# Kernel tuning notes

Hardware: AMD Instinct MI355X
Metric: run time of the kernel (lower is better)

## Reference

```python
import jax, jax.numpy as jnp
import numpy as np

N_TOK = 256
C_Z = 128
C = 32
N_HEAD = 4


def setup_inputs() -> dict:
    key = jax.random.key(0)
    ks = jax.random.split(key, 8)
    s = 0.02
    return {
        "z": jax.random.normal(ks[0], (N_TOK, N_TOK, C_Z), dtype=jnp.float32),
        "single_mask": jnp.ones((N_TOK,), dtype=jnp.float32),
        "ln_gamma": jnp.ones((C_Z,), dtype=jnp.float32),
        "ln_beta": jnp.zeros((C_Z,), dtype=jnp.float32),
        "W_q": jax.random.normal(ks[1], (C_Z, N_HEAD * C), dtype=jnp.float32) * s,
        "W_k": jax.random.normal(ks[2], (C_Z, N_HEAD * C), dtype=jnp.float32) * s,
        "W_v": jax.random.normal(ks[3], (C_Z, N_HEAD * C), dtype=jnp.float32) * s,
        "W_b": jax.random.normal(ks[4], (C_Z, N_HEAD), dtype=jnp.float32) * s,
        "W_g": jax.random.normal(ks[5], (C_Z, N_HEAD * C), dtype=jnp.float32) * s,
        "W_out": jax.random.normal(ks[6], (N_HEAD * C, C_Z), dtype=jnp.float32) * s,
    }


def reference(z, single_mask, ln_gamma, ln_beta, W_q, W_k, W_v, W_b, W_g, W_out):
    # LayerNorm over c_z
    mu = jnp.mean(z, axis=-1, keepdims=True)
    var = jnp.var(z, axis=-1, keepdims=True)
    zn = (z - mu) * jax.lax.rsqrt(var + 1e-5) * ln_gamma + ln_beta

    n = zn.shape[0]
    proj = lambda W: (zn @ W).reshape(n, n, N_HEAD, C)
    q = proj(W_q)
    k = proj(W_k)
    v = proj(W_v)
    g = proj(W_g)
    b = zn @ W_b  # [i, j, h] -> used as bias b[j, k, h]

    # a[i,j,k,h] = q[i,j]·k[i,k]/sqrt(c) + b[j,k,h]
    a = jnp.einsum('ijhc,ikhc->ijkh', q, k) / np.sqrt(C).astype(np.float32)
    a = a + b[None, :, :, :]
    a = a + (-1e9) * (1.0 - single_mask)[None, None, :, None]
    a = jax.nn.softmax(a, axis=-2)  # over k

    o = jnp.einsum('ijkh,ikhc->ijhc', a, v)
    o = jax.nn.sigmoid(g) * o
    o = o.reshape(n, n, N_HEAD * C)
    return o @ W_out
```

## Files before the change

kernel.cpp:

```cpp
#include <hip/hip_runtime.h>
#include <hip/hip_bf16.h>

#define NT 256
#define CZ 128
#define CH 32
#define NH 4
#define PL 2097152

typedef unsigned short ushort_t;
typedef unsigned int uint_t;
typedef __attribute__((ext_vector_type(8))) short short8;
typedef __attribute__((ext_vector_type(4))) float f32x4;

__device__ __forceinline__ float bfbits2f(uint_t bits){
  union { uint_t u; float f; } v; v.u = bits; return v.f;
}
__device__ __forceinline__ float bf2f(ushort_t u){
  return bfbits2f(((uint_t)u) << 16);
}
__device__ __forceinline__ ushort_t f2bf(float f){
  union { float f; uint_t u; } v; v.f = f;
  uint_t u = v.u;
  uint_t r = (u + 0x7fffu + ((u >> 16) & 1u)) >> 16;
  return (ushort_t)r;
}
__device__ __forceinline__ void unpk(uint_t w, float& lo, float& hi){
  lo = bfbits2f(w << 16);
  hi = bfbits2f(w & 0xffff0000u);
}
__device__ __forceinline__ short8 as_s8(uint4 u){
  union { uint4 u; short8 s; } v; v.u = u; return v.s;
}
__device__ __forceinline__ uint_t pk2(float a, float b){
  union { __hip_bfloat16 h; ushort_t u; } x, y;
  x.h = __float2bfloat16(a); y.h = __float2bfloat16(b);
  return (uint_t)x.u | ((uint_t)y.u << 16);
}
__device__ __forceinline__ int detect_f32(const ushort_t* zz){
  int l = threadIdx.x & 63;
  int bad = 0;
  #pragma unroll
  for(int s=0;s<4;s++){
    float v = bf2f(zz[l*4 + s]);
    if(!(fabsf(v) < 1e9f)) bad = 1;
  }
  return (__ballot(bad) != 0ull) ? 1 : 0;
}

__global__ __launch_bounds__(256) void k_cvt_wt(const void* __restrict__ s0,
    const void* __restrict__ s1, const void* __restrict__ s2,
    const void* __restrict__ s3, const void* __restrict__ s4,
    ushort_t* __restrict__ dst, const ushort_t* __restrict__ zz,
    const void* __restrict__ m_, const void* __restrict__ g_,
    const void* __restrict__ b_, const void* __restrict__ wb_,
    float* __restrict__ smallf){
  int isf32 = detect_f32(zz);
  if(blockIdx.x >= 320){
    int idx = threadIdx.x * 4;
    const void* sp; int off;
    if(idx < 256){ sp = m_;  off = idx; }
    else if(idx < 384){ sp = g_;  off = idx-256; }
    else if(idx < 512){ sp = b_;  off = idx-384; }
    else { sp = wb_; off = idx-512; }
    float4 o;
    if(isf32){ o = *(const float4*)((const float*)sp + off); }
    else {
      uint2 u = *(const uint2*)((const ushort_t*)sp + off);
      unpk(u.x, o.x, o.y); unpk(u.y, o.z, o.w);
    }
    *(float4*)(smallf + idx) = o;
    return;
  }
  const void* srcs[5] = {s0,s1,s2,s3,s4};
  int w = blockIdx.x >> 6;
  int idx = (blockIdx.x & 63)*256 + threadIdx.x;
  int k = idx >> 7, c = idx & 127;
  const void* sp = srcs[w];
  float v;
  if(isf32) v = ((const float*)sp)[idx];
  else      v = bf2f(((const ushort_t*)sp)[idx]);
  dst[(size_t)w*16384 + (size_t)c*128 + k] = f2bf(v);
}

__global__ __launch_bounds__(256) void k_lnproj(const void* __restrict__ zraw,
    const float* __restrict__ smallf, const ushort_t* __restrict__ Wt,
    ushort_t* __restrict__ qh, ushort_t* __restrict__ kh,
    ushort_t* __restrict__ vh, ushort_t* __restrict__ gh,
    float* __restrict__ btm){
  __shared__ __align__(16) char lds[37888];
  ushort_t* znl = (ushort_t*)lds;
  float*    wbs = (float*)(lds + 35840);
  const float* mkf = smallf;
  const float* gmf = smallf + 256;
  const float* btf = smallf + 384;
  const float* Wbf = smallf + 512;
  int t = threadIdx.x;
  int isf32 = detect_f32((const ushort_t*)zraw);
  wbs[t] = Wbf[t]; wbs[t+256] = Wbf[t+256];
  __syncthreads();

  int row_loc = t >> 1, half = t & 1;
  size_t r = (size_t)blockIdx.x*128 + row_loc;
  float mval = -1e9f * (1.f - mkf[r & 255]);
  float s = 0.f, s2 = 0.f;
  if(isf32){
    const float4* zp = (const float4*)((const float*)zraw + r*CZ + half*64);
    #pragma unroll
    for(int q=0;q<16;q++){
      float4 v = zp[q];
      s  += (v.x + v.y) + (v.z + v.w);
      s2 += (v.x*v.x + v.y*v.y) + (v.z*v.z + v.w*v.w);
    }
  } else {
    const uint4* zp = (const uint4*)((const ushort_t*)zraw + r*CZ + half*64);
    #pragma unroll
    for(int q=0;q<8;q++){
      uint4 u = zp[q];
      const uint_t* pu = (const uint_t*)&u;
      #pragma unroll
      for(int e=0;e<4;e++){
        float lo, hi; unpk(pu[e], lo, hi);
        s += lo + hi; s2 += lo*lo + hi*hi;
      }
    }
  }
  s  += __shfl_xor(s, 1);
  s2 += __shfl_xor(s2, 1);
  float mu  = s * (1.f/CZ);
  float var = fmaxf(s2 * (1.f/CZ) - mu*mu, 0.f);
  float rs  = rsqrtf(var + 1e-5f);
  float acch[4] = {0.f,0.f,0.f,0.f};
  #pragma unroll
  for(int chunk=0;chunk<8;chunk++){
    float v8[8];
    if(isf32){
      const float4* zp = (const float4*)((const float*)zraw + r*CZ + half*64 + chunk*8);
      float4 a = zp[0], b = zp[1];
      v8[0]=a.x; v8[1]=a.y; v8[2]=a.z; v8[3]=a.w;
      v8[4]=b.x; v8[5]=b.y; v8[6]=b.z; v8[7]=b.w;
    } else {
      uint4 u = *(const uint4*)((const ushort_t*)zraw + r*CZ + half*64 + chunk*8);
      const uint_t* pu = (const uint_t*)&u;
      #pragma unroll
      for(int e=0;e<4;e++) unpk(pu[e], v8[e*2], v8[e*2+1]);
    }
    uint_t ow[4];
    #pragma unroll
    for(int e2=0;e2<4;e2++){
      int cg = half*64 + chunk*8 + e2*2;
      float v0 = (v8[e2*2]   - mu)*rs*gmf[cg]   + btf[cg];
      float v1 = (v8[e2*2+1] - mu)*rs*gmf[cg+1] + btf[cg+1];
      float4 w0 = *(const float4*)&wbs[cg*4];
      float4 w1 = *(const float4*)&wbs[(cg+1)*4];
      acch[0] += v0*w0.x + v1*w1.x;
      acch[1] += v0*w0.y + v1*w1.y;
      acch[2] += v0*w0.z + v1*w1.z;
      acch[3] += v0*w0.w + v1*w1.w;
      ow[e2] = (uint_t)f2bf(v0) | ((uint_t)f2bf(v1) << 16);
    }
    uint4 o; o.x=ow[0]; o.y=ow[1]; o.z=ow[2]; o.w=ow[3];
    *(uint4*)(znl + row_loc*140 + half*64 + chunk*8) = o;
  }
  #pragma unroll
  for(int h=0;h<4;h++){
    float tot = acch[h] + __shfl_xor(acch[h], 1);
    if(half == 0) btm[(size_t)h*65536 + r] = (tot + mval) * 1.4426950408889634f;
  }
  __syncthreads();

  int wave = t>>6, l = t&63, n = l&15, quad = l>>4;
  uint4 af[2][4];
  #pragma unroll
  for(int mt=0;mt<2;mt++)
    #pragma unroll
    for(int kb=0;kb<4;kb++)
      af[mt][kb] = *(const uint4*)(znl + (wave*32 + mt*16 + n)*140 + kb*32 + quad*8);
  ushort_t* outs[4] = {qh, kh, vh, gh};
  size_t row0 = (size_t)blockIdx.x*128 + wave*32;
  #pragma unroll
  for(int w=0;w<4;w++){
    const ushort_t* W = Wt + (size_t)w*16384;
    ushort_t* D = outs[w];
    float sc = (w==0) ? (0.17677669529663687f * 1.4426950408889634f) : 1.f;
    #pragma unroll
    for(int nt=0;nt<8;nt++){
      uint4 bfr[4];
      #pragma unroll
      for(int kb=0;kb<4;kb++)
        bfr[kb] = *(const uint4*)(W + ((size_t)(nt*16 + n))*128 + kb*32 + quad*8);
      f32x4 a0 = {0.f,0.f,0.f,0.f}, a1 = {0.f,0.f,0.f,0.f};
      #pragma unroll
      for(int kb=0;kb<4;kb++){
        a0 = __builtin_amdgcn_mfma_f32_16x16x32_bf16(as_s8(bfr[kb]), as_s8(af[0][kb]), a0, 0,0,0);
        a1 = __builtin_amdgcn_mfma_f32_16x16x32_bf16(as_s8(bfr[kb]), as_s8(af[1][kb]), a1, 0,0,0);
      }
      uint2 s0p, s1p;
      s0p.x = pk2(a0[0]*sc, a0[1]*sc); s0p.y = pk2(a0[2]*sc, a0[3]*sc);
      s1p.x = pk2(a1[0]*sc, a1[1]*sc); s1p.y = pk2(a1[2]*sc, a1[3]*sc);
      ushort_t* Db = D + (size_t)(nt>>1)*PL + (size_t)(nt&1)*16 + quad*4;
      *(uint2*)(Db + (row0 + n)*CH)      = s0p;
      *(uint2*)(Db + (row0 + 16 + n)*CH) = s1p;
    }
  }
}

__global__ __launch_bounds__(512, 2) void k_attn(
    const ushort_t* __restrict__ qh, const ushort_t* __restrict__ kh,
    const ushort_t* __restrict__ vh, const ushort_t* __restrict__ gh,
    const float* __restrict__ btm, ushort_t* __restrict__ oh,
    const ushort_t* __restrict__ Wt4, void* __restrict__ outp,
    const ushort_t* __restrict__ zz){
  __shared__ __align__(16) char lds[147456];
  int t = threadIdx.x;
  int i = blockIdx.x;
  int w = t >> 6, l = t & 63;
  int h = w >> 1, sub = w & 1;
  int n = l & 15, quad = l >> 4;
  uint4*    Kf  = (uint4*)(lds + h*16384);
  uint4*    VfA = (uint4*)(lds + 65536 + h*16384);
  ushort_t* Pw  = (ushort_t*)(lds + 131072) + w*1024;
  const ushort_t* qhp = qh + (size_t)h*PL + (size_t)(i*NT)*CH;
  const ushort_t* khp = kh + (size_t)h*PL + (size_t)(i*NT)*CH;
  const ushort_t* vhp = vh + (size_t)h*PL + (size_t)(i*NT)*CH;
  const ushort_t* ghp = gh + (size_t)h*PL + (size_t)(i*NT)*CH;
  ushort_t*       ohp = oh + (size_t)h*PL + (size_t)(i*NT)*CH;
  const float*    bth = btm + (size_t)h*65536;

  {
    #pragma unroll
    for(int m=0;m<8;m++){
      int kt = sub*8 + m;
      Kf[kt*64 + l] = *(const uint4*)(khp + (size_t)(kt*16 + n)*CH + quad*8);
    }
  }
  {
    #pragma unroll
    for(int it=0; it<8; it++){
      int u = sub + it*2, kblk = u >> 1, ct = u & 1;
      uint_t d[4];
      #pragma unroll
      for(int e=0;e<4;e++){
        uint_t lo = vhp[(size_t)(kblk*32 + quad*8 + e*2    )*CH + ct*16 + n];
        uint_t hi = vhp[(size_t)(kblk*32 + quad*8 + e*2 + 1)*CH + ct*16 + n];
        d[e] = lo | (hi << 16);
      }
      uint4 o; o.x=d[0]; o.y=d[1]; o.z=d[2]; o.w=d[3];
      VfA[u*64 + l] = o;
    }
  }
  __syncthreads();

  int swz = (n & 7) << 4;

  #pragma unroll 1
  for(int s=0;s<8;s++){
    int jt = sub*8 + s;
    uint4 qf = *(const uint4*)(qhp + (size_t)(jt*16 + n)*CH + quad*8);
    f32x4 acc[16];
    #pragma unroll
    for(int kt=0;kt<16;kt++)
      acc[kt] = *(const f32x4*)(bth + (size_t)(jt*16 + n)*256 + kt*16 + quad*4);
    #pragma unroll
    for(int kt=0;kt<16;kt++){
      uint4 kfv = Kf[kt*64 + l];
      acc[kt] = __builtin_amdgcn_mfma_f32_16x16x32_bf16(as_s8(kfv), as_s8(qf), acc[kt], 0,0,0);
    }
    float sum0 = 0.f, sum1 = 0.f;
    f32x4 oa0 = {0.f,0.f,0.f,0.f}, oa1 = {0.f,0.f,0.f,0.f};
    #pragma unroll
    for(int H=0;H<2;H++){
      uint2 pv[8];
      #pragma unroll
      for(int kt=0;kt<8;kt++){
        float e0 = __builtin_amdgcn_exp2f(acc[H*8+kt][0]);
        float e1 = __builtin_amdgcn_exp2f(acc[H*8+kt][1]);
        float e2 = __builtin_amdgcn_exp2f(acc[H*8+kt][2]);
        float e3 = __builtin_amdgcn_exp2f(acc[H*8+kt][3]);
        sum0 += e0 + e1; sum1 += e2 + e3;
        pv[kt].x = pk2(e0, e1);
        pv[kt].y = pk2(e2, e3);
      }
      #pragma unroll
      for(int Q2=0;Q2<2;Q2++){
        #pragma unroll
        for(int m=0;m<4;m++)
          *(uint2*)((char*)Pw + (((n<<7) + (m<<5) + (quad<<3)) ^ swz)) = pv[Q2*4+m];
        #pragma unroll
        for(int kb=0;kb<2;kb++){
          uint4 pf = *(const uint4*)((char*)Pw + (((n<<7) + (kb<<6) + (quad<<4)) ^ swz));
          int kg = (H*2+Q2)*2 + kb;
          oa0 = __builtin_amdgcn_mfma_f32_16x16x32_bf16(as_s8(VfA[(kg*2+0)*64 + l]), as_s8(pf), oa0, 0,0,0);
          oa1 = __builtin_amdgcn_mfma_f32_16x16x32_bf16(as_s8(VfA[(kg*2+1)*64 + l]), as_s8(pf), oa1, 0,0,0);
        }
      }
    }
    float ssum = sum0 + sum1;
    ssum += __shfl_xor(ssum, 16);
    ssum += __shfl_xor(ssum, 32);
    float inv = 1.f / ssum;
    size_t rb = (size_t)(jt*16 + n)*CH;
    uint2 g0 = *(const uint2*)(ghp + rb + quad*4);
    uint2 g1 = *(const uint2*)(ghp + rb + 16 + quad*4);
    float ga[4], gc[4];
    unpk(g0.x, ga[0], ga[1]); unpk(g0.y, ga[2], ga[3]);
    unpk(g1.x, gc[0], gc[1]); unpk(g1.y, gc[2], gc[3]);
    float v0[4], v1[4];
    #pragma unroll
    for(int rr=0;rr<4;rr++){
      v0[rr] = oa0[rr] * inv * (1.f/(1.f + __expf(-ga[rr])));
      v1[rr] = oa1[rr] * inv * (1.f/(1.f + __expf(-gc[rr])));
    }
    uint2 s0, s1;
    s0.x = (uint_t)f2bf(v0[0]) | ((uint_t)f2bf(v0[1]) << 16);
    s0.y = (uint_t)f2bf(v0[2]) | ((uint_t)f2bf(v0[3]) << 16);
    s1.x = (uint_t)f2bf(v1[0]) | ((uint_t)f2bf(v1[1]) << 16);
    s1.y = (uint_t)f2bf(v1[2]) | ((uint_t)f2bf(v1[3]) << 16);
    *(uint2*)(ohp + rb + quad*4)      = s0;
    *(uint2*)(ohp + rb + 16 + quad*4) = s1;
  }
  __syncthreads();

  int isf32 = detect_f32(zz);
  size_t row0 = (size_t)i*NT + w*32;
  uint4 af[2][4];
  #pragma unroll
  for(int mt=0;mt<2;mt++)
    #pragma unroll
    for(int kb=0;kb<4;kb++)
      af[mt][kb] = *(const uint4*)(oh + (size_t)kb*PL + (row0 + mt*16 + n)*CH + quad*8);
  #pragma unroll
  for(int nt=0;nt<8;nt++){
    uint4 bfr[4];
    #pragma unroll
    for(int kb=0;kb<4;kb++)
      bfr[kb] = *(const uint4*)(Wt4 + ((size_t)(nt*16 + n))*128 + kb*32 + quad*8);
    f32x4 a0 = {0.f,0.f,0.f,0.f}, a1 = {0.f,0.f,0.f,0.f};
    #pragma unroll
    for(int kb=0;kb<4;kb++){
      a0 = __builtin_amdgcn_mfma_f32_16x16x32_bf16(as_s8(bfr[kb]), as_s8(af[0][kb]), a0, 0,0,0);
      a1 = __builtin_amdgcn_mfma_f32_16x16x32_bf16(as_s8(bfr[kb]), as_s8(af[1][kb]), a1, 0,0,0);
    }
    if(isf32){
      float* of = (float*)outp + nt*16 + quad*4;
      *(f32x4*)(of + (row0 + n)*CZ)      = a0;
      *(f32x4*)(of + (row0 + 16 + n)*CZ) = a1;
    } else {
      uint2 s0p, s1p;
      s0p.x = pk2(a0[0], a0[1]); s0p.y = pk2(a0[2], a0[3]);
      s1p.x = pk2(a1[0], a1[1]); s1p.y = pk2(a1[2], a1[3]);
      ushort_t* ob = (ushort_t*)outp + nt*16 + quad*4;
      *(uint2*)(ob + (row0 + n)*CZ)      = s0p;
      *(uint2*)(ob + (row0 + 16 + n)*CZ) = s1p;
    }
  }
}

extern "C" void kernel_launch(void* const* d_in, const int* in_sizes, int n_in,
                              void* d_out, int out_size, void* d_ws, size_t ws_size,
                              hipStream_t stream){
  char* wsb = (char*)d_ws;
  const size_t TB = (size_t)16777216;
  ushort_t* qh  = (ushort_t*)(wsb);
  ushort_t* kh  = (ushort_t*)(wsb + TB);
  ushort_t* vh  = (ushort_t*)(wsb + 2*TB);
  ushort_t* gh  = (ushort_t*)(wsb + 3*TB);
  ushort_t* oh  = (ushort_t*)(wsb + 4*TB);
  float*    btm = (float*)   (wsb + 5*TB);
  float*  smallf= (float*)   (wsb + 5*TB + (1u<<20));
  ushort_t* Wt  = (ushort_t*)(wsb + 5*TB + (1u<<20) + 4096);
  const ushort_t* zz = (const ushort_t*)d_in[0];

  k_cvt_wt   <<<321, 256, 0, stream>>>(d_in[4], d_in[5], d_in[6], d_in[8], d_in[9],
                                       Wt, zz, d_in[1], d_in[2], d_in[3], d_in[7], smallf);
  k_lnproj   <<<512, 256, 0, stream>>>(d_in[0], smallf, Wt, qh, kh, vh, gh, btm);
  k_attn     <<<256, 512, 0, stream>>>(qh, kh, vh, gh, btm, oh,
                                       Wt + (size_t)4*16384, d_out, zz);
}
```

Baseline: 197.5 us.

## Fuse LN and QKVG projection into attention kernel; split bias via folded LN algebra

After: 206.8 us. 1.05x slower.

```diff
diff --git a/kernel.cpp b/kernel.cpp
--- a/kernel.cpp
+++ b/kernel.cpp
@@ -53,7 +53,7 @@
     ushort_t* __restrict__ dst, const ushort_t* __restrict__ zz,
     const void* __restrict__ m_, const void* __restrict__ g_,
     const void* __restrict__ b_, const void* __restrict__ wb_,
-    float* __restrict__ smallf){
+    float* __restrict__ smallf, float* __restrict__ abct){
   int isf32 = detect_f32(zz);
   if(blockIdx.x >= 320){
     int idx = threadIdx.x * 4;
@@ -69,6 +69,21 @@
       unpk(u.x, o.x, o.y); unpk(u.y, o.z, o.w);
     }
     *(float4*)(smallf + idx) = o;
+    __syncthreads();
+    if(threadIdx.x < 128){
+      int c = threadIdx.x;
+      float g = smallf[256 + c];
+      #pragma unroll
+      for(int h=0;h<4;h++) abct[c*4 + h] = g * smallf[512 + c*4 + h];
+    }
+    if(threadIdx.x >= 128 && threadIdx.x < 136){
+      int k = threadIdx.x - 128;
+      int h = k & 3, which = k >> 2;
+      float acc = 0.f;
+      for(int c=0;c<128;c++)
+        acc += (which ? smallf[256 + c] : smallf[384 + c]) * smallf[512 + c*4 + h];
+      abct[512 + k] = acc;
+    }
     return;
   }
   const void* srcs[5] = {s0,s1,s2,s3,s4};
@@ -82,27 +97,21 @@
   dst[(size_t)w*16384 + (size_t)c*128 + k] = f2bf(v);
 }
 
-__global__ __launch_bounds__(256) void k_lnproj(const void* __restrict__ zraw,
-    const float* __restrict__ smallf, const ushort_t* __restrict__ Wt,
-    ushort_t* __restrict__ qh, ushort_t* __restrict__ kh,
-    ushort_t* __restrict__ vh, ushort_t* __restrict__ gh,
+__global__ __launch_bounds__(256) void k_bias(const void* __restrict__ zraw,
+    const float* __restrict__ smallf, const float* __restrict__ abct,
     float* __restrict__ btm){
-  __shared__ __align__(16) char lds[37888];
-  ushort_t* znl = (ushort_t*)lds;
-  float*    wbs = (float*)(lds + 35840);
-  const float* mkf = smallf;
-  const float* gmf = smallf + 256;
-  const float* btf = smallf + 384;
-  const float* Wbf = smallf + 512;
+  __shared__ float As[512];
+  __shared__ float BC[8];
   int t = threadIdx.x;
   int isf32 = detect_f32((const ushort_t*)zraw);
-  wbs[t] = Wbf[t]; wbs[t+256] = Wbf[t+256];
+  As[t] = abct[t]; As[t+256] = abct[t+256];
+  if(t < 8) BC[t] = abct[512 + t];
   __syncthreads();
-
   int row_loc = t >> 1, half = t & 1;
   size_t r = (size_t)blockIdx.x*128 + row_loc;
-  float mval = -1e9f * (1.f - mkf[r & 255]);
-  float s = 0.f, s2 = 0.f;
+  float mval = -1e9f * (1.f - smallf[r & 255]);
+  float s = 0.f, s2 = 0.f, d[4] = {0.f,0.f,0.f,0.f};
+  const float* Ah = As + half*256;
   if(isf32){
     const float4* zp = (const float4*)((const float*)zraw + r*CZ + half*64);
     #pragma unroll
@@ -110,6 +119,10 @@
       float4 v = zp[q];
       s  += (v.x + v.y) + (v.z + v.w);
       s2 += (v.x*v.x + v.y*v.y) + (v.z*v.z + v.w*v.w);
+      const float* a0 = Ah + q*16;
+      #pragma unroll
+      for(int h=0;h<4;h++)
+        d[h] += v.x*a0[h] + v.y*a0[4+h] + v.z*a0[8+h] + v.w*a0[12+h];
     }
   } else {
     const uint4* zp = (const uint4*)((const ushort_t*)zraw + r*CZ + half*64);
@@ -121,101 +134,139 @@
       for(int e=0;e<4;e++){
         float lo, hi; unpk(pu[e], lo, hi);
         s += lo + hi; s2 += lo*lo + hi*hi;
+        const float* a0 = Ah + (q*8 + e*2)*4;
+        #pragma unroll
+        for(int h=0;h<4;h++) d[h] += lo*a0[h] + hi*a0[4+h];
       }
     }
   }
   s  += __shfl_xor(s, 1);
   s2 += __shfl_xor(s2, 1);
-  float mu  = s * (1.f/CZ);
-  float var = fmaxf(s2 * (1.f/CZ) - mu*mu, 0.f);
-  float rs  = rsqrtf(var + 1e-5f);
-  float acch[4] = {0.f,0.f,0.f,0.f};
   #pragma unroll
-  for(int chunk=0;chunk<8;chunk++){
-    float v8[8];
-    if(isf32){
-      const float4* zp = (const float4*)((const float*)zraw + r*CZ + half*64 + chunk*8);
-      float4 a = zp[0], b = zp[1];
-      v8[0]=a.x; v8[1]=a.y; v8[2]=a.z; v8[3]=a.w;
-      v8[4]=b.x; v8[5]=b.y; v8[6]=b.z; v8[7]=b.w;
-    } else {
-      uint4 u = *(const uint4*)((const ushort_t*)zraw + r*CZ + half*64 + chunk*8);
-      const uint_t* pu = (const uint_t*)&u;
-      #pragma unroll
-      for(int e=0;e<4;e++) unpk(pu[e], v8[e*2], v8[e*2+1]);
-    }
-    uint_t ow[4];
-    #pragma unroll
-    for(int e2=0;e2<4;e2++){
-      int cg = half*64 + chunk*8 + e2*2;
-      float v0 = (v8[e2*2]   - mu)*rs*gmf[cg]   + btf[cg];
-      float v1 = (v8[e2*2+1] - mu)*rs*gmf[cg+1] + btf[cg+1];
-      float4 w0 = *(const float4*)&wbs[cg*4];
-      float4 w1 = *(const float4*)&wbs[(cg+1)*4];
-      acch[0] += v0*w0.x + v1*w1.x;
-      acch[1] += v0*w0.y + v1*w1.y;
-      acch[2] += v0*w0.z + v1*w1.z;
-      acch[3] += v0*w0.w + v1*w1.w;
-      ow[e2] = (uint_t)f2bf(v0) | ((uint_t)f2bf(v1) << 16);
-    }
-    uint4 o; o.x=ow[0]; o.y=ow[1]; o.z=ow[2]; o.w=ow[3];
-    *(uint4*)(znl + row_loc*140 + half*64 + chunk*8) = o;
-  }
-  #pragma unroll
-  for(int h=0;h<4;h++){
-    float tot = acch[h] + __shfl_xor(acch[h], 1);
-    if(half == 0) btm[(size_t)h*65536 + r] = (tot + mval) * 1.4426950408889634f;
-  }
-  __syncthreads();
-
-  int wave = t>>6, l = t&63, n = l&15, quad = l>>4;
-  uint4 af[2][4];
-  #pragma unroll
-  for(int mt=0;mt<2;mt++)
-    #pragma unroll
-    for(int kb=0;kb<4;kb++)
-      af[mt][kb] = *(const uint4*)(znl + (wave*32 + mt*16 + n)*140 + kb*32 + quad*8);
-  ushort_t* outs[4] = {qh, kh, vh, gh};
-  size_t row0 = (size_t)blockIdx.x*128 + wave*32;
-  #pragma unroll
-  for(int w=0;w<4;w++){
-    const ushort_t* W = Wt + (size_t)w*16384;
-    ushort_t* D = outs[w];
-    float sc = (w==0) ? (0.17677669529663687f * 1.4426950408889634f) : 1.f;
-    #pragma unroll
-    for(int nt=0;nt<8;nt++){
-      uint4 bfr[4];
-      #pragma unroll
-      for(int kb=0;kb<4;kb++)
-        bfr[kb] = *(const uint4*)(W + ((size_t)(nt*16 + n))*128 + kb*32 + quad*8);
-      f32x4 a0 = {0.f,0.f,0.f,0.f}, a1 = {0.f,0.f,0.f,0.f};
-      #pragma unroll
-      for(int kb=0;kb<4;kb++){
-        a0 = __builtin_amdgcn_mfma_f32_16x16x32_bf16(as_s8(bfr[kb]), as_s8(af[0][kb]), a0, 0,0,0);
-        a1 = __builtin_amdgcn_mfma_f32_16x16x32_bf16(as_s8(bfr[kb]), as_s8(af[1][kb]), a1, 0,0,0);
-      }
-      uint2 s0p, s1p;
-      s0p.x = pk2(a0[0]*sc, a0[1]*sc); s0p.y = pk2(a0[2]*sc, a0[3]*sc);
-      s1p.x = pk2(a1[0]*sc, a1[1]*sc); s1p.y = pk2(a1[2]*sc, a1[3]*sc);
-      ushort_t* Db = D + (size_t)(nt>>1)*PL + (size_t)(nt&1)*16 + quad*4;
-      *(uint2*)(Db + (row0 + n)*CH)      = s0p;
-      *(uint2*)(Db + (row0 + 16 + n)*CH) = s1p;
-    }
-  }
-}
-
-__global__ __launch_bounds__(512, 2) void k_attn(
-    const ushort_t* __restrict__ qh, const ushort_t* __restrict__ kh,
-    const ushort_t* __restrict__ vh, const ushort_t* __restrict__ gh,
+  for(int h=0;h<4;h++) d[h] += __shfl_xor(d[h], 1);
+  if(half == 0){
+    float mu  = s * (1.f/CZ);
+    float var = fmaxf(s2 * (1.f/CZ) - mu*mu, 0.f);
+    float rs  = rsqrtf(var + 1e-5f);
+    #pragma unroll
+    for(int h=0;h<4;h++){
+      float bias = rs*(d[h] - mu*BC[4+h]) + BC[h];
+      btm[(size_t)h*65536 + r] = (bias + mval) * 1.4426950408889634f;
+    }
+  }
+}
+
+__global__ __launch_bounds__(512) void k_fused(const void* __restrict__ zraw,
+    const float* __restrict__ smallf, const ushort_t* __restrict__ Wt,
+    ushort_t* __restrict__ qh, ushort_t* __restrict__ kh,
+    ushort_t* __restrict__ vh, ushort_t* __restrict__ gh,
     const float* __restrict__ btm, ushort_t* __restrict__ oh,
-    const ushort_t* __restrict__ Wt4, void* __restrict__ outp,
-    const ushort_t* __restrict__ zz){
+    void* __restrict__ outp){
   __shared__ __align__(16) char lds[147456];
+  ushort_t* znl = (ushort_t*)lds;
   int t = threadIdx.x;
   int i = blockIdx.x;
-  int w = t >> 6, l = t & 63;
+  int isf32 = detect_f32((const ushort_t*)zraw);
+  const float* gmf = smallf + 256;
+  const float* btf = smallf + 384;
+
+  {
+    int row_loc = t >> 1, half = t & 1;
+    size_t r = (size_t)i*256 + row_loc;
+    float s = 0.f, s2 = 0.f;
+    if(isf32){
+      const float4* zp = (const float4*)((const float*)zraw + r*CZ + half*64);
+      #pragma unroll
+      for(int q=0;q<16;q++){
+        float4 v = zp[q];
+        s  += (v.x + v.y) + (v.z + v.w);
+        s2 += (v.x*v.x + v.y*v.y) + (v.z*v.z + v.w*v.w);
+      }
+    } else {
+      const uint4* zp = (const uint4*)((const ushort_t*)zraw + r*CZ + half*64);
+      #pragma unroll
+      for(int q=0;q<8;q++){
+        uint4 u = zp[q];
+        const uint_t* pu = (const uint_t*)&u;
+        #pragma unroll
+        for(int e=0;e<4;e++){
+          float lo, hi; unpk(pu[e], lo, hi);
+          s += lo + hi; s2 += lo*lo + hi*hi;
+        }
+      }
+    }
+    s  += __shfl_xor(s, 1);
+    s2 += __shfl_xor(s2, 1);
+    float mu  = s * (1.f/CZ);
+    float var = fmaxf(s2 * (1.f/CZ) - mu*mu, 0.f);
+    float rs  = rsqrtf(var + 1e-5f);
+    #pragma unroll
+    for(int chunk=0;chunk<8;chunk++){
+      float v8[8];
+      if(isf32){
+        const float4* zp = (const float4*)((const float*)zraw + r*CZ + half*64 + chunk*8);
+        float4 a = zp[0], b = zp[1];
+        v8[0]=a.x; v8[1]=a.y; v8[2]=a.z; v8[3]=a.w;
+        v8[4]=b.x; v8[5]=b.y; v8[6]=b.z; v8[7]=b.w;
+      } else {
+        uint4 u = *(const uint4*)((const ushort_t*)zraw + r*CZ + half*64 + chunk*8);
+        const uint_t* pu = (const uint_t*)&u;
+        #pragma unroll
+        for(int e=0;e<4;e++) unpk(pu[e], v8[e*2], v8[e*2+1]);
+      }
+      uint_t ow[4];
+      #pragma unroll
+      for(int e2=0;e2<4;e2++){
+        int cg = half*64 + chunk*8 + e2*2;
+        float v0 = (v8[e2*2]   - mu)*rs*gmf[cg]   + btf[cg];
+        float v1 = (v8[e2*2+1] - mu)*rs*gmf[cg+1] + btf[cg+1];
+        ow[e2] = (uint_t)f2bf(v0) | ((uint_t)f2bf(v1) << 16);
+      }
+      uint4 o; o.x=ow[0]; o.y=ow[1]; o.z=ow[2]; o.w=ow[3];
+      *(uint4*)(znl + row_loc*140 + half*64 + chunk*8) = o;
+    }
+  }
+  __syncthreads();
+
+  int w = t >> 6, l = t & 63, n = l & 15, quad = l >> 4;
+  {
+    uint4 af[2][4];
+    #pragma unroll
+    for(int mt=0;mt<2;mt++)
+      #pragma unroll
+      for(int kb=0;kb<4;kb++)
+        af[mt][kb] = *(const uint4*)(znl + (w*32 + mt*16 + n)*140 + kb*32 + quad*8);
+    ushort_t* outs[4] = {qh, kh, vh, gh};
+    size_t row0 = (size_t)i*256 + w*32;
+    #pragma unroll
+    for(int ww=0;ww<4;ww++){
+      const ushort_t* W = Wt + (size_t)ww*16384;
+      ushort_t* D = outs[ww];
+      float sc = (ww==0) ? (0.17677669529663687f * 1.4426950408889634f) : 1.f;
+      #pragma unroll
+      for(int nt=0;nt<8;nt++){
+        uint4 bfr[4];
+        #pragma unroll
+        for(int kb=0;kb<4;kb++)
+          bfr[kb] = *(const uint4*)(W + ((size_t)(nt*16 + n))*128 + kb*32 + quad*8);
+        f32x4 a0 = {0.f,0.f,0.f,0.f}, a1 = {0.f,0.f,0.f,0.f};
+        #pragma unroll
+        for(int kb=0;kb<4;kb++){
+          a0 = __builtin_amdgcn_mfma_f32_16x16x32_bf16(as_s8(bfr[kb]), as_s8(af[0][kb]), a0, 0,0,0);
+          a1 = __builtin_amdgcn_mfma_f32_16x16x32_bf16(as_s8(bfr[kb]), as_s8(af[1][kb]), a1, 0,0,0);
+        }
+        uint2 s0p, s1p;
+        s0p.x = pk2(a0[0]*sc, a0[1]*sc); s0p.y = pk2(a0[2]*sc, a0[3]*sc);
+        s1p.x = pk2(a1[0]*sc, a1[1]*sc); s1p.y = pk2(a1[2]*sc, a1[3]*sc);
+        ushort_t* Db = D + (size_t)(nt>>1)*PL + (size_t)(nt&1)*16 + quad*4;
+        *(uint2*)(Db + (row0 + n)*CH)      = s0p;
+        *(uint2*)(Db + (row0 + 16 + n)*CH) = s1p;
+      }
+    }
+  }
+  __syncthreads();
+
   int h = w >> 1, sub = w & 1;
-  int n = l & 15, quad = l >> 4;
   uint4*    Kf  = (uint4*)(lds + h*16384);
   uint4*    VfA = (uint4*)(lds + 65536 + h*16384);
   ushort_t* Pw  = (ushort_t*)(lds + 131072) + w*1024;
@@ -311,46 +362,46 @@
       v1[rr] = oa1[rr] * inv * (1.f/(1.f + __expf(-gc[rr])));
     }
     uint2 s0, s1;
-    s0.x = (uint_t)f2bf(v0[0]) | ((uint_t)f2bf(v0[1]) << 16);
-    s0.y = (uint_t)f2bf(v0[2]) | ((uint_t)f2bf(v0[3]) << 16);
-    s1.x = (uint_t)f2bf(v1[0]) | ((uint_t)f2bf(v1[1]) << 16);
-    s1.y = (uint_t)f2bf(v1[2]) | ((uint_t)f2bf(v1[3]) << 16);
+    s0.x = pk2(v0[0], v0[1]); s0.y = pk2(v0[2], v0[3]);
+    s1.x = pk2(v1[0], v1[1]); s1.y = pk2(v1[2], v1[3]);
     *(uint2*)(ohp + rb + quad*4)      = s0;
     *(uint2*)(ohp + rb + 16 + quad*4) = s1;
   }
   __syncthreads();
 
-  int isf32 = detect_f32(zz);
-  size_t row0 = (size_t)i*NT + w*32;
-  uint4 af[2][4];
-  #pragma unroll
-  for(int mt=0;mt<2;mt++)
-    #pragma unroll
-    for(int kb=0;kb<4;kb++)
-      af[mt][kb] = *(const uint4*)(oh + (size_t)kb*PL + (row0 + mt*16 + n)*CH + quad*8);
-  #pragma unroll
-  for(int nt=0;nt<8;nt++){
-    uint4 bfr[4];
-    #pragma unroll
-    for(int kb=0;kb<4;kb++)
-      bfr[kb] = *(const uint4*)(Wt4 + ((size_t)(nt*16 + n))*128 + kb*32 + quad*8);
-    f32x4 a0 = {0.f,0.f,0.f,0.f}, a1 = {0.f,0.f,0.f,0.f};
-    #pragma unroll
-    for(int kb=0;kb<4;kb++){
-      a0 = __builtin_amdgcn_mfma_f32_16x16x32_bf16(as_s8(bfr[kb]), as_s8(af[0][kb]), a0, 0,0,0);
-      a1 = __builtin_amdgcn_mfma_f32_16x16x32_bf16(as_s8(bfr[kb]), as_s8(af[1][kb]), a1, 0,0,0);
-    }
-    if(isf32){
-      float* of = (float*)outp + nt*16 + quad*4;
-      *(f32x4*)(of + (row0 + n)*CZ)      = a0;
-      *(f32x4*)(of + (row0 + 16 + n)*CZ) = a1;
-    } else {
-      uint2 s0p, s1p;
-      s0p.x = pk2(a0[0], a0[1]); s0p.y = pk2(a0[2], a0[3]);
-      s1p.x = pk2(a1[0], a1[1]); s1p.y = pk2(a1[2], a1[3]);
-      ushort_t* ob = (ushort_t*)outp + nt*16 + quad*4;
-      *(uint2*)(ob + (row0 + n)*CZ)      = s0p;
-      *(uint2*)(ob + (row0 + 16 + n)*CZ) = s1p;
+  {
+    const ushort_t* Wt4 = Wt + (size_t)4*16384;
+    size_t row0 = (size_t)i*NT + w*32;
+    uint4 af[2][4];
+    #pragma unroll
+    for(int mt=0;mt<2;mt++)
+      #pragma unroll
+      for(int kb=0;kb<4;kb++)
+        af[mt][kb] = *(const uint4*)(oh + (size_t)kb*PL + (row0 + mt*16 + n)*CH + quad*8);
+    #pragma unroll
+    for(int nt=0;nt<8;nt++){
+      uint4 bfr[4];
+      #pragma unroll
+      for(int kb=0;kb<4;kb++)
+        bfr[kb] = *(const uint4*)(Wt4 + ((size_t)(nt*16 + n))*128 + kb*32 + quad*8);
+      f32x4 a0 = {0.f,0.f,0.f,0.f}, a1 = {0.f,0.f,0.f,0.f};
+      #pragma unroll
+      for(int kb=0;kb<4;kb++){
+        a0 = __builtin_amdgcn_mfma_f32_16x16x32_bf16(as_s8(bfr[kb]), as_s8(af[0][kb]), a0, 0,0,0);
+        a1 = __builtin_amdgcn_mfma_f32_16x16x32_bf16(as_s8(bfr[kb]), as_s8(af[1][kb]), a1, 0,0,0);
+      }
+      if(isf32){
+        float* of = (float*)outp + nt*16 + quad*4;
+        *(f32x4*)(of + (row0 + n)*CZ)      = a0;
+        *(f32x4*)(of + (row0 + 16 + n)*CZ) = a1;
+      } else {
+        uint2 s0p, s1p;
+        s0p.x = pk2(a0[0], a0[1]); s0p.y = pk2(a0[2], a0[3]);
+        s1p.x = pk2(a1[0], a1[1]); s1p.y = pk2(a1[2], a1[3]);
+        ushort_t* ob = (ushort_t*)outp + nt*16 + quad*4;
+        *(uint2*)(ob + (row0 + n)*CZ)      = s0p;
+        *(uint2*)(ob + (row0 + 16 + n)*CZ) = s1p;
+      }
     }
   }
 }
@@ -368,11 +419,13 @@
   float*    btm = (float*)   (wsb + 5*TB);
   float*  smallf= (float*)   (wsb + 5*TB + (1u<<20));
   ushort_t* Wt  = (ushort_t*)(wsb + 5*TB + (1u<<20) + 4096);
+  float*   abct = (float*)   (wsb + 5*TB + (1u<<20) + 4096 + 163840);
   const ushort_t* zz = (const ushort_t*)d_in[0];
 
-  k_cvt_wt   <<<321, 256, 0, stream>>>(d_in[4], d_in[5], d_in[6], d_in[8], d_in[9],
-                                       Wt, zz, d_in[1], d_in[2], d_in[3], d_in[7], smallf);
-  k_lnproj   <<<512, 256, 0, stream>>>(d_in[0], smallf, Wt, qh, kh, vh, gh, btm);
-  k_attn     <<<256, 512, 0, stream>>>(qh, kh, vh, gh, btm, oh,
-                                       Wt + (size_t)4*16384, d_out, zz);
-}
+  k_cvt_wt <<<321, 256, 0, stream>>>(d_in[4], d_in[5], d_in[6], d_in[8], d_in[9],
+                                     Wt, zz, d_in[1], d_in[2], d_in[3], d_in[7],
+                                     smallf, abct);
+  k_bias   <<<512, 256, 0, stream>>>(d_in[0], smallf, abct, btm);
+  k_fused  <<<256, 512, 0, stream>>>(d_in[0], smallf, Wt, qh, kh, vh, gh,
+                                     btm, oh, d_out);
+}
```

## Fuse LN/projection and attention kernels with a global atomic grid barrier

Applied to the files above, without the earlier changes.

New measurement: 311.6 us. 57.8% more time.

```diff
diff --git a/kernel.cpp b/kernel.cpp
--- a/kernel.cpp
+++ b/kernel.cpp
@@ -82,140 +82,143 @@
   dst[(size_t)w*16384 + (size_t)c*128 + k] = f2bf(v);
 }
 
-__global__ __launch_bounds__(256) void k_lnproj(const void* __restrict__ zraw,
+__global__ __launch_bounds__(512) void k_fused(const void* __restrict__ zraw,
     const float* __restrict__ smallf, const ushort_t* __restrict__ Wt,
     ushort_t* __restrict__ qh, ushort_t* __restrict__ kh,
     ushort_t* __restrict__ vh, ushort_t* __restrict__ gh,
-    float* __restrict__ btm){
-  __shared__ __align__(16) char lds[37888];
+    float* __restrict__ btm, ushort_t* __restrict__ oh,
+    void* __restrict__ outp, uint_t* __restrict__ ctr){
+  __shared__ __align__(16) char lds[147456];
   ushort_t* znl = (ushort_t*)lds;
-  float*    wbs = (float*)(lds + 35840);
+  float*    wbs = (float*)(lds + 71680);
+  int t = threadIdx.x;
+  int i = blockIdx.x;
+  int isf32 = detect_f32((const ushort_t*)zraw);
   const float* mkf = smallf;
   const float* gmf = smallf + 256;
   const float* btf = smallf + 384;
   const float* Wbf = smallf + 512;
-  int t = threadIdx.x;
-  int isf32 = detect_f32((const ushort_t*)zraw);
-  wbs[t] = Wbf[t]; wbs[t+256] = Wbf[t+256];
-  __syncthreads();
-
-  int row_loc = t >> 1, half = t & 1;
-  size_t r = (size_t)blockIdx.x*128 + row_loc;
-  float mval = -1e9f * (1.f - mkf[r & 255]);
-  float s = 0.f, s2 = 0.f;
-  if(isf32){
-    const float4* zp = (const float4*)((const float*)zraw + r*CZ + half*64);
-    #pragma unroll
-    for(int q=0;q<16;q++){
-      float4 v = zp[q];
-      s  += (v.x + v.y) + (v.z + v.w);
-      s2 += (v.x*v.x + v.y*v.y) + (v.z*v.z + v.w*v.w);
-    }
-  } else {
-    const uint4* zp = (const uint4*)((const ushort_t*)zraw + r*CZ + half*64);
-    #pragma unroll
-    for(int q=0;q<8;q++){
-      uint4 u = zp[q];
-      const uint_t* pu = (const uint_t*)&u;
-      #pragma unroll
-      for(int e=0;e<4;e++){
-        float lo, hi; unpk(pu[e], lo, hi);
-        s += lo + hi; s2 += lo*lo + hi*hi;
-      }
-    }
-  }
-  s  += __shfl_xor(s, 1);
-  s2 += __shfl_xor(s2, 1);
-  float mu  = s * (1.f/CZ);
-  float var = fmaxf(s2 * (1.f/CZ) - mu*mu, 0.f);
-  float rs  = rsqrtf(var + 1e-5f);
-  float acch[4] = {0.f,0.f,0.f,0.f};
-  #pragma unroll
-  for(int chunk=0;chunk<8;chunk++){
-    float v8[8];
+  wbs[t] = Wbf[t & 511];
+  __syncthreads();
+
+  {
+    int row_loc = t >> 1, half = t & 1;
+    size_t r = (size_t)i*256 + row_loc;
+    float mval = -1e9f * (1.f - mkf[r & 255]);
+    float s = 0.f, s2 = 0.f;
     if(isf32){
-      const float4* zp = (const float4*)((const float*)zraw + r*CZ + half*64 + chunk*8);
-      float4 a = zp[0], b = zp[1];
-      v8[0]=a.x; v8[1]=a.y; v8[2]=a.z; v8[3]=a.w;
-      v8[4]=b.x; v8[5]=b.y; v8[6]=b.z; v8[7]=b.w;
+      const float4* zp = (const float4*)((const float*)zraw + r*CZ + half*64);
+      #pragma unroll
+      for(int q=0;q<16;q++){
+        float4 v = zp[q];
+        s  += (v.x + v.y) + (v.z + v.w);
+        s2 += (v.x*v.x + v.y*v.y) + (v.z*v.z + v.w*v.w);
+      }
     } else {
-      uint4 u = *(const uint4*)((const ushort_t*)zraw + r*CZ + half*64 + chunk*8);
-      const uint_t* pu = (const uint_t*)&u;
-      #pragma unroll
-      for(int e=0;e<4;e++) unpk(pu[e], v8[e*2], v8[e*2+1]);
-    }
-    uint_t ow[4];
-    #pragma unroll
-    for(int e2=0;e2<4;e2++){
-      int cg = half*64 + chunk*8 + e2*2;
-      float v0 = (v8[e2*2]   - mu)*rs*gmf[cg]   + btf[cg];
-      float v1 = (v8[e2*2+1] - mu)*rs*gmf[cg+1] + btf[cg+1];
-      float4 w0 = *(const float4*)&wbs[cg*4];
-      float4 w1 = *(const float4*)&wbs[(cg+1)*4];
-      acch[0] += v0*w0.x + v1*w1.x;
-      acch[1] += v0*w0.y + v1*w1.y;
-      acch[2] += v0*w0.z + v1*w1.z;
-      acch[3] += v0*w0.w + v1*w1.w;
-      ow[e2] = (uint_t)f2bf(v0) | ((uint_t)f2bf(v1) << 16);
-    }
-    uint4 o; o.x=ow[0]; o.y=ow[1]; o.z=ow[2]; o.w=ow[3];
-    *(uint4*)(znl + row_loc*140 + half*64 + chunk*8) = o;
-  }
-  #pragma unroll
-  for(int h=0;h<4;h++){
-    float tot = acch[h] + __shfl_xor(acch[h], 1);
-    if(half == 0) btm[(size_t)h*65536 + r] = (tot + mval) * 1.4426950408889634f;
-  }
-  __syncthreads();
-
-  int wave = t>>6, l = t&63, n = l&15, quad = l>>4;
-  uint4 af[2][4];
-  #pragma unroll
-  for(int mt=0;mt<2;mt++)
-    #pragma unroll
-    for(int kb=0;kb<4;kb++)
-      af[mt][kb] = *(const uint4*)(znl + (wave*32 + mt*16 + n)*140 + kb*32 + quad*8);
-  ushort_t* outs[4] = {qh, kh, vh, gh};
-  size_t row0 = (size_t)blockIdx.x*128 + wave*32;
-  #pragma unroll
-  for(int w=0;w<4;w++){
-    const ushort_t* W = Wt + (size_t)w*16384;
-    ushort_t* D = outs[w];
-    float sc = (w==0) ? (0.17677669529663687f * 1.4426950408889634f) : 1.f;
-    #pragma unroll
-    for(int nt=0;nt<8;nt++){
-      uint4 bfr[4];
+      const uint4* zp = (const uint4*)((const ushort_t*)zraw + r*CZ + half*64);
+      #pragma unroll
+      for(int q=0;q<8;q++){
+        uint4 u = zp[q];
+        const uint_t* pu = (const uint_t*)&u;
+        #pragma unroll
+        for(int e=0;e<4;e++){
+          float lo, hi; unpk(pu[e], lo, hi);
+          s += lo + hi; s2 += lo*lo + hi*hi;
+        }
+      }
+    }
+    s  += __shfl_xor(s, 1);
+    s2 += __shfl_xor(s2, 1);
+    float mu  = s * (1.f/CZ);
+    float var = fmaxf(s2 * (1.f/CZ) - mu*mu, 0.f);
+    float rs  = rsqrtf(var + 1e-5f);
+    float acch[4] = {0.f,0.f,0.f,0.f};
+    #pragma unroll
+    for(int chunk=0;chunk<8;chunk++){
+      float v8[8];
+      if(isf32){
+        const float4* zp = (const float4*)((const float*)zraw + r*CZ + half*64 + chunk*8);
+        float4 a = zp[0], b = zp[1];
+        v8[0]=a.x; v8[1]=a.y; v8[2]=a.z; v8[3]=a.w;
+        v8[4]=b.x; v8[5]=b.y; v8[6]=b.z; v8[7]=b.w;
+      } else {
+        uint4 u = *(const uint4*)((const ushort_t*)zraw + r*CZ + half*64 + chunk*8);
+        const uint_t* pu = (const uint_t*)&u;
+        #pragma unroll
+        for(int e=0;e<4;e++) unpk(pu[e], v8[e*2], v8[e*2+1]);
+      }
+      uint_t ow[4];
+      #pragma unroll
+      for(int e2=0;e2<4;e2++){
+        int cg = half*64 + chunk*8 + e2*2;
+        float v0 = (v8[e2*2]   - mu)*rs*gmf[cg]   + btf[cg];
+        float v1 = (v8[e2*2+1] - mu)*rs*gmf[cg+1] + btf[cg+1];
+        float4 w0 = *(const float4*)&wbs[cg*4];
+        float4 w1 = *(const float4*)&wbs[(cg+1)*4];
+        acch[0] += v0*w0.x + v1*w1.x;
+        acch[1] += v0*w0.y + v1*w1.y;
+        acch[2] += v0*w0.z + v1*w1.z;
+        acch[3] += v0*w0.w + v1*w1.w;
+        ow[e2] = (uint_t)f2bf(v0) | ((uint_t)f2bf(v1) << 16);
+      }
+      uint4 o; o.x=ow[0]; o.y=ow[1]; o.z=ow[2]; o.w=ow[3];
+      *(uint4*)(znl + row_loc*140 + half*64 + chunk*8) = o;
+    }
+    #pragma unroll
+    for(int hh=0;hh<4;hh++){
+      float tot = acch[hh] + __shfl_xor(acch[hh], 1);
+      if(half == 0) btm[(size_t)hh*65536 + r] = (tot + mval) * 1.4426950408889634f;
+    }
+  }
+  __syncthreads();
+
+  int w = t >> 6, l = t & 63, n = l & 15, quad = l >> 4;
+  {
+    uint4 af[2][4];
+    #pragma unroll
+    for(int mt=0;mt<2;mt++)
       #pragma unroll
       for(int kb=0;kb<4;kb++)
-        bfr[kb] = *(const uint4*)(W + ((size_t)(nt*16 + n))*128 + kb*32 + quad*8);
-      f32x4 a0 = {0.f,0.f,0.f,0.f}, a1 = {0.f,0.f,0.f,0.f};
-      #pragma unroll
-      for(int kb=0;kb<4;kb++){
-        a0 = __builtin_amdgcn_mfma_f32_16x16x32_bf16(as_s8(bfr[kb]), as_s8(af[0][kb]), a0, 0,0,0);
-        a1 = __builtin_amdgcn_mfma_f32_16x16x32_bf16(as_s8(bfr[kb]), as_s8(af[1][kb]), a1, 0,0,0);
-      }
-      uint2 s0p, s1p;
-      s0p.x = pk2(a0[0]*sc, a0[1]*sc); s0p.y = pk2(a0[2]*sc, a0[3]*sc);
-      s1p.x = pk2(a1[0]*sc, a1[1]*sc); s1p.y = pk2(a1[2]*sc, a1[3]*sc);
-      ushort_t* Db = D + (size_t)(nt>>1)*PL + (size_t)(nt&1)*16 + quad*4;
-      *(uint2*)(Db + (row0 + n)*CH)      = s0p;
-      *(uint2*)(Db + (row0 + 16 + n)*CH) = s1p;
-    }
-  }
-}
-
-__global__ __launch_bounds__(512, 2) void k_attn(
-    const ushort_t* __restrict__ qh, const ushort_t* __restrict__ kh,
-    const ushort_t* __restrict__ vh, const ushort_t* __restrict__ gh,
-    const float* __restrict__ btm, ushort_t* __restrict__ oh,
-    const ushort_t* __restrict__ Wt4, void* __restrict__ outp,
-    const ushort_t* __restrict__ zz){
-  __shared__ __align__(16) char lds[147456];
-  int t = threadIdx.x;
-  int i = blockIdx.x;
-  int w = t >> 6, l = t & 63;
+        af[mt][kb] = *(const uint4*)(znl + (w*32 + mt*16 + n)*140 + kb*32 + quad*8);
+    ushort_t* outs[4] = {qh, kh, vh, gh};
+    size_t row0 = (size_t)i*256 + w*32;
+    #pragma unroll
+    for(int ww=0;ww<4;ww++){
+      const ushort_t* W = Wt + (size_t)ww*16384;
+      ushort_t* D = outs[ww];
+      float sc = (ww==0) ? (0.17677669529663687f * 1.4426950408889634f) : 1.f;
+      #pragma unroll
+      for(int nt=0;nt<8;nt++){
+        uint4 bfr[4];
+        #pragma unroll
+        for(int kb=0;kb<4;kb++)
+          bfr[kb] = *(const uint4*)(W + ((size_t)(nt*16 + n))*128 + kb*32 + quad*8);
+        f32x4 a0 = {0.f,0.f,0.f,0.f}, a1 = {0.f,0.f,0.f,0.f};
+        #pragma unroll
+        for(int kb=0;kb<4;kb++){
+          a0 = __builtin_amdgcn_mfma_f32_16x16x32_bf16(as_s8(bfr[kb]), as_s8(af[0][kb]), a0, 0,0,0);
+          a1 = __builtin_amdgcn_mfma_f32_16x16x32_bf16(as_s8(bfr[kb]), as_s8(af[1][kb]), a1, 0,0,0);
+        }
+        uint2 s0p, s1p;
+        s0p.x = pk2(a0[0]*sc, a0[1]*sc); s0p.y = pk2(a0[2]*sc, a0[3]*sc);
+        s1p.x = pk2(a1[0]*sc, a1[1]*sc); s1p.y = pk2(a1[2]*sc, a1[3]*sc);
+        ushort_t* Db = D + (size_t)(nt>>1)*PL + (size_t)(nt&1)*16 + quad*4;
+        *(uint2*)(Db + (row0 + n)*CH)      = s0p;
+        *(uint2*)(Db + (row0 + 16 + n)*CH) = s1p;
+      }
+    }
+  }
+
+  __syncthreads();
+  if(t == 0){
+    __threadfence();
+    __hip_atomic_fetch_add(ctr, 1u, __ATOMIC_ACQ_REL, __HIP_MEMORY_SCOPE_AGENT);
+    while(__hip_atomic_load(ctr, __ATOMIC_ACQUIRE, __HIP_MEMORY_SCOPE_AGENT) < 256u){}
+  }
+  __syncthreads();
+  __threadfence();
+
   int h = w >> 1, sub = w & 1;
-  int n = l & 15, quad = l >> 4;
   uint4*    Kf  = (uint4*)(lds + h*16384);
   uint4*    VfA = (uint4*)(lds + 65536 + h*16384);
   ushort_t* Pw  = (ushort_t*)(lds + 131072) + w*1024;
@@ -311,46 +314,46 @@
       v1[rr] = oa1[rr] * inv * (1.f/(1.f + __expf(-gc[rr])));
     }
     uint2 s0, s1;
-    s0.x = (uint_t)f2bf(v0[0]) | ((uint_t)f2bf(v0[1]) << 16);
-    s0.y = (uint_t)f2bf(v0[2]) | ((uint_t)f2bf(v0[3]) << 16);
-    s1.x = (uint_t)f2bf(v1[0]) | ((uint_t)f2bf(v1[1]) << 16);
-    s1.y = (uint_t)f2bf(v1[2]) | ((uint_t)f2bf(v1[3]) << 16);
+    s0.x = pk2(v0[0], v0[1]); s0.y = pk2(v0[2], v0[3]);
+    s1.x = pk2(v1[0], v1[1]); s1.y = pk2(v1[2], v1[3]);
     *(uint2*)(ohp + rb + quad*4)      = s0;
     *(uint2*)(ohp + rb + 16 + quad*4) = s1;
   }
   __syncthreads();
 
-  int isf32 = detect_f32(zz);
-  size_t row0 = (size_t)i*NT + w*32;
-  uint4 af[2][4];
-  #pragma unroll
-  for(int mt=0;mt<2;mt++)
-    #pragma unroll
-    for(int kb=0;kb<4;kb++)
-      af[mt][kb] = *(const uint4*)(oh + (size_t)kb*PL + (row0 + mt*16 + n)*CH + quad*8);
-  #pragma unroll
-  for(int nt=0;nt<8;nt++){
-    uint4 bfr[4];
-    #pragma unroll
-    for(int kb=0;kb<4;kb++)
-      bfr[kb] = *(const uint4*)(Wt4 + ((size_t)(nt*16 + n))*128 + kb*32 + quad*8);
-    f32x4 a0 = {0.f,0.f,0.f,0.f}, a1 = {0.f,0.f,0.f,0.f};
-    #pragma unroll
-    for(int kb=0;kb<4;kb++){
-      a0 = __builtin_amdgcn_mfma_f32_16x16x32_bf16(as_s8(bfr[kb]), as_s8(af[0][kb]), a0, 0,0,0);
-      a1 = __builtin_amdgcn_mfma_f32_16x16x32_bf16(as_s8(bfr[kb]), as_s8(af[1][kb]), a1, 0,0,0);
-    }
-    if(isf32){
-      float* of = (float*)outp + nt*16 + quad*4;
-      *(f32x4*)(of + (row0 + n)*CZ)      = a0;
-      *(f32x4*)(of + (row0 + 16 + n)*CZ) = a1;
-    } else {
-      uint2 s0p, s1p;
-      s0p.x = pk2(a0[0], a0[1]); s0p.y = pk2(a0[2], a0[3]);
-      s1p.x = pk2(a1[0], a1[1]); s1p.y = pk2(a1[2], a1[3]);
-      ushort_t* ob = (ushort_t*)outp + nt*16 + quad*4;
-      *(uint2*)(ob + (row0 + n)*CZ)      = s0p;
-      *(uint2*)(ob + (row0 + 16 + n)*CZ) = s1p;
+  {
+    const ushort_t* Wt4 = Wt + (size_t)4*16384;
+    size_t row0 = (size_t)i*NT + w*32;
+    uint4 af[2][4];
+    #pragma unroll
+    for(int mt=0;mt<2;mt++)
+      #pragma unroll
+      for(int kb=0;kb<4;kb++)
+        af[mt][kb] = *(const uint4*)(oh + (size_t)kb*PL + (row0 + mt*16 + n)*CH + quad*8);
+    #pragma unroll
+    for(int nt=0;nt<8;nt++){
+      uint4 bfr[4];
+      #pragma unroll
+      for(int kb=0;kb<4;kb++)
+        bfr[kb] = *(const uint4*)(Wt4 + ((size_t)(nt*16 + n))*128 + kb*32 + quad*8);
+      f32x4 a0 = {0.f,0.f,0.f,0.f}, a1 = {0.f,0.f,0.f,0.f};
+      #pragma unroll
+      for(int kb=0;kb<4;kb++){
+        a0 = __builtin_amdgcn_mfma_f32_16x16x32_bf16(as_s8(bfr[kb]), as_s8(af[0][kb]), a0, 0,0,0);
+        a1 = __builtin_amdgcn_mfma_f32_16x16x32_bf16(as_s8(bfr[kb]), as_s8(af[1][kb]), a1, 0,0,0);
+      }
+      if(isf32){
+        float* of = (float*)outp + nt*16 + quad*4;
+        *(f32x4*)(of + (row0 + n)*CZ)      = a0;
+        *(f32x4*)(of + (row0 + 16 + n)*CZ) = a1;
+      } else {
+        uint2 s0p, s1p;
+        s0p.x = pk2(a0[0], a0[1]); s0p.y = pk2(a0[2], a0[3]);
+        s1p.x = pk2(a1[0], a1[1]); s1p.y = pk2(a1[2], a1[3]);
+        ushort_t* ob = (ushort_t*)outp + nt*16 + quad*4;
+        *(uint2*)(ob + (row0 + n)*CZ)      = s0p;
+        *(uint2*)(ob + (row0 + 16 + n)*CZ) = s1p;
+      }
     }
   }
 }
@@ -368,11 +371,13 @@
   float*    btm = (float*)   (wsb + 5*TB);
   float*  smallf= (float*)   (wsb + 5*TB + (1u<<20));
   ushort_t* Wt  = (ushort_t*)(wsb + 5*TB + (1u<<20) + 4096);
+  uint_t*   ctr = (uint_t*)  (wsb + 5*TB + (1u<<20) + 4096 + 163840);
   const ushort_t* zz = (const ushort_t*)d_in[0];
 
-  k_cvt_wt   <<<321, 256, 0, stream>>>(d_in[4], d_in[5], d_in[6], d_in[8], d_in[9],
-                                       Wt, zz, d_in[1], d_in[2], d_in[3], d_in[7], smallf);
-  k_lnproj   <<<512, 256, 0, stream>>>(d_in[0], smallf, Wt, qh, kh, vh, gh, btm);
-  k_attn     <<<256, 512, 0, stream>>>(qh, kh, vh, gh, btm, oh,
-                                       Wt + (size_t)4*16384, d_out, zz);
-}
+  hipMemsetAsync(ctr, 0, 4, stream);
+  k_cvt_wt <<<321, 256, 0, stream>>>(d_in[4], d_in[5], d_in[6], d_in[8], d_in[9],
+                                     Wt, zz, d_in[1], d_in[2], d_in[3], d_in[7],
+                                     smallf);
+  k_fused  <<<256, 512, 0, stream>>>(d_in[0], smallf, Wt, qh, kh, vh, gh,
+                                     btm, oh, d_out, ctr);
+}
```
